# Performance work log

Measured on AMD Instinct MI355X. Metric: run time of the kernel, lower is better.

## Reference

```python
import jax, jax.numpy as jnp
import numpy as np

B, T, F = 128, 256, 6      # batch, input_seq_len, input feature dim
H, L = 512, 4              # hidden_size, hidden_layers
S, D = 32, 3               # output_seq_len, output_dim


def setup_inputs() -> dict:
    key = jax.random.key(0)
    ks = jax.random.split(key, 8)
    sc = 0.05
    x = jax.random.normal(ks[0], (B, T, F), dtype=jnp.float32)
    centre = jnp.zeros((F,), dtype=jnp.float32)          # uniform_centre
    bound = jnp.ones((F,), dtype=jnp.float32)            # uniform_bound
    W0 = jax.random.normal(ks[1], (F, 4 * H), dtype=jnp.float32) * sc   # layer0 kernel
    Wk = jax.random.normal(ks[2], (L - 1, H, 4 * H), dtype=jnp.float32) * sc  # layers 1..L-1 kernels
    U = jax.random.normal(ks[3], (L, H, 4 * H), dtype=jnp.float32) * sc # recurrent kernels
    b = jnp.zeros((L, 4 * H), dtype=jnp.float32)
    Wd = jax.random.normal(ks[4], (H, D), dtype=jnp.float32) * sc       # dense kernel
    bd = jnp.zeros((D,), dtype=jnp.float32)
    return {"x": x, "centre": centre, "bound": bound, "W0": W0,
            "Wk": Wk, "U": U, "b": b, "Wd": Wd, "bd": bd}


def _lstm_layer(x_tbf, W, U, b):
    """Keras LSTMCell over time-major input [T, B, Fin] -> [T, B, H]."""
    xW = jnp.einsum('tbf,fh->tbh', x_tbf, W)  # precompute input projections
    Bn = x_tbf.shape[1]
    Hn = U.shape[0]
    h0 = jnp.zeros((Bn, Hn), dtype=x_tbf.dtype)

    def step(carry, xw):
        h, c = carry
        z = xw + h @ U + b  # [B, 4H], keras gate order: i, f, g(c), o
        i, f, g, o = jnp.split(z, 4, axis=-1)
        i = jax.nn.sigmoid(i)
        f = jax.nn.sigmoid(f)
        g = jnp.tanh(g)
        o = jax.nn.sigmoid(o)
        c = f * c + i * g
        h = o * jnp.tanh(c)
        return (h, c), h

    _, hs = jax.lax.scan(step, (h0, h0), xW)
    return hs


def reference(x, centre, bound, W0, Wk, U, b, Wd, bd):
    # UniformDiff: uniform-scale then first difference along time (axis 1)
    u = (x - centre) / bound                 # [B, T, F]
    d = u[:, 1:, :] - u[:, :-1, :]           # [B, T-1, F]
    seq = jnp.transpose(d, (1, 0, 2))        # time-major [T-1, B, F]
    # stacked LSTM (generic RNN over StackedRNNCells)
    seq = _lstm_layer(seq, W0, U[0], b[0])
    for l in range(1, L):
        seq = _lstm_layer(seq, Wk[l - 1], U[l], b[l])
    h = jnp.transpose(seq, (1, 0, 2))        # [B, T-1, H]
    out = h[:, -S:, :] @ Wd + bd             # [B, S, D]
    # Restore: invert uniform scaling on the first D features
    pred = out * bound[:D] + centre[:D]
    return (out, pred)
```

## Files before the change

kernel.cpp:

```cpp
#include <hip/hip_runtime.h>
#include <cstdint>
#include <cstddef>


typedef __bf16 bf16x8  __attribute__((ext_vector_type(8)));
typedef float  f32x4   __attribute__((ext_vector_type(4)));
typedef float  f32x16  __attribute__((ext_vector_type(16)));
typedef unsigned int u32x4 __attribute__((ext_vector_type(4)));

#define STG_SLOT  262144ull
#define STG_L     65536ull
#define STG_MG    32768ull
#define STG_CG    1024ull

#define RING_SLOT 32768ull
#define RING_MG   (8ull*RING_SLOT)
#define RING_L    (2ull*RING_MG)
#define SZ_RING   (4ull*RING_L*2ull)

#define OFF_STG  0ull
#define SZ_STG   (256ull*STG_SLOT*2ull)
#define OFF_D    (OFF_STG + SZ_STG)
#define SZ_D     524288ull
#define OFF_BIAS (OFF_D + SZ_D)
#define SZ_BIAS  32768ull
#define OFF_FLAG (OFF_BIAS + SZ_BIAS)
#define SZ_FLAG  32768ull
#define OFF_FFLAG (OFF_FLAG + SZ_FLAG)
#define SZ_FFLAG 32768ull
#define OFF_RING (OFF_FFLAG + SZ_FFLAG)
#define OFF_BP   (OFF_RING + SZ_RING)
#define NK16_L0  33
#define BPE_L0   (64ull*NK16_L0*64ull*8ull)
#define BPE_STR  (64ull*64ull*64ull*8ull)

#define LDS_ZPAD   72
#define LDS_ZBYTES 18432
#define LDS_WBYTES 131072
#define LDS_TOTAL  (LDS_ZBYTES + LDS_WBYTES)

#define VMWAIT(N) do { asm volatile("s_waitcnt vmcnt(" #N ")" ::: "memory"); \
                       __builtin_amdgcn_sched_barrier(0); } while (0)

__device__ __forceinline__ void gld16(u32x4& d, const unsigned short* p) {
    asm volatile("global_load_dwordx4 %0, %1, off" : "=v"(d) : "v"(p));
}
__device__ __forceinline__ void gld16_sc0(u32x4& d, const unsigned short* p) {
    asm volatile("global_load_dwordx4 %0, %1, off sc0" : "=v"(d) : "v"(p));
}
__device__ __forceinline__ int ld_fast(const int* p) {
    int v;
    asm volatile("global_load_dword %0, %1, off sc0\n\t"
                 "s_waitcnt vmcnt(0)" : "=v"(v) : "v"(p) : "memory");
    return v;
}
__device__ __forceinline__ int ld_slow(const int* p) {
    return __hip_atomic_load(p, __ATOMIC_RELAXED, __HIP_MEMORY_SCOPE_AGENT);
}
__device__ __forceinline__ void ld_slow_async(int& v, const int* p) {
    asm volatile("global_load_dword %0, %1, off sc0 sc1" : "=v"(v) : "v"(p));
}

__device__ __forceinline__ unsigned short f2bf(float f) {
    unsigned int u = __builtin_bit_cast(unsigned int, f);
    unsigned int lsb = (u >> 16) & 1u;
    u += 0x7fffu + lsb;
    return (unsigned short)(u >> 16);
}
__device__ __forceinline__ float bf2f(unsigned short s) {
    unsigned int u = ((unsigned int)s) << 16;
    return __builtin_bit_cast(float, u);
}
__device__ __forceinline__ float fsig(float x)  { return 1.0f / (1.0f + __expf(-x)); }
__device__ __forceinline__ float ftanh(float x) { float e = __expf(2.0f * x); return 1.0f - 2.0f / (e + 1.0f); }

__global__ void prep_bias(const float* __restrict__ b, float* __restrict__ bias_ws) {
    int idx = blockIdx.x * 256 + threadIdx.x;
    if (idx >= 4 * 2048) return;
    int l = idx >> 11, c = idx & 2047;
    int j = ((c >> 6) << 4) + (c & 15);
    int gate = (c >> 4) & 3;
    bias_ws[idx] = b[l * 2048 + gate * 512 + j];
}

__global__ void prep_bp32(int layer, int NK16,
                          const float* __restrict__ W0, const float* __restrict__ Wk,
                          const float* __restrict__ U, unsigned short* __restrict__ bp) {
    int idx = blockIdx.x * 256 + threadIdx.x;
    int total = 64 * NK16 * 64;
    if (idx >= total) return;
    int lane = idx & 63;
    int rest = idx >> 6;
    int ks = rest % NK16;
    int ct = rest / NK16;
    int c = ct * 32 + (lane & 31);
    int j = ((c >> 6) << 4) + (c & 15);
    int gate = (c >> 4) & 3;
    int sc = gate * 512 + j;
    int kbase = ks * 16 + ((lane >> 5) << 3);
    unsigned short outv[8];
#pragma unroll
    for (int i = 0; i < 8; i++) {
        int k = kbase + i;
        float v = 0.0f;
        if (layer == 0) {
            if (k < 8) { if (k < 6) v = W0[(size_t)k * 2048 + sc]; }
            else if (k < 520) v = U[(size_t)(k - 8) * 2048 + sc];
        } else {
            if (k < 512) v = Wk[((size_t)(layer - 1) * 512 + k) * 2048 + sc];
            else         v = U[((size_t)layer * 512 + (k - 512)) * 2048 + sc];
        }
        outv[i] = f2bf(v);
    }
    *(uint4*)(bp + (size_t)idx * 8) = *(const uint4*)outv;
}

__global__ void diffk(const float* __restrict__ x, const float* __restrict__ bound,
                      unsigned short* __restrict__ dbuf) {
    int idx = blockIdx.x * 256 + threadIdx.x;
    if (idx >= 255 * 128) return;
    int item = idx & 127, t = idx >> 7;
    const float* xr = x + ((size_t)item * 256 + t) * 6;
    unsigned short row[8];
#pragma unroll
    for (int f = 0; f < 6; f++) row[f] = f2bf((xr[6 + f] - xr[f]) / bound[f]);
    row[6] = 0; row[7] = 0;
    *(uint4*)(dbuf + (size_t)idx * 8) = *(const uint4*)row;
}

__global__ __launch_bounds__(256, 1) void lstm_persist(
    const unsigned short* __restrict__ dbuf,
    unsigned short* __restrict__ stg,
    unsigned short* __restrict__ ring,
    const unsigned short* __restrict__ bp_all,
    const float* __restrict__ bias,
    int* __restrict__ slowf,
    int* __restrict__ fastf)
{
    extern __shared__ char smem[];
    float* zsm = (float*)smem;
    unsigned short* wsm = (unsigned short*)(smem + LDS_ZBYTES);

    (void)__hip_atomic_load(&slowf[0], __ATOMIC_ACQUIRE, __HIP_MEMORY_SCOPE_AGENT);

    const int blk   = blockIdx.x;
    const int stage = blk & 7;
    const int layer = stage >> 1;
    const int mg    = stage & 1;
    const int cg    = blk >> 3;
    const int tid   = threadIdx.x;
    const int w     = tid >> 6;
    const int lane  = tid & 63;
    const int NK16  = (layer == 0) ? NK16_L0 : 64;

    {
        const unsigned short* src = bp_all
            + (layer == 0 ? 0ull : (BPE_L0 + (size_t)(layer - 1) * BPE_STR))
            + (size_t)(cg * 2) * NK16 * 64 * 8;
        int nv = 2 * NK16 * 64;
        for (int e = tid; e < nv; e += 256)
            ((uint4*)wsm)[e] = ((const uint4*)src)[e];
    }
    __syncthreads();

    const int mt    = w >> 1;
    const int ntl   = w & 1;
    const int khalf = lane >> 5;
    const int arow  = mg * 64 + mt * 32 + (lane & 31);
    const int aloc  = arow & 63;
    const unsigned short* wbase = wsm + (size_t)ntl * NK16 * 512 + (size_t)lane * 8;
    const int citem = tid >> 2;
    const int jsub  = (tid & 3) << 2;
    const f32x4 bI = *(const f32x4*)(bias + layer * 2048 + cg * 64 + 0  + jsub);
    const f32x4 bF = *(const f32x4*)(bias + layer * 2048 + cg * 64 + 16 + jsub);
    const f32x4 bG = *(const f32x4*)(bias + layer * 2048 + cg * 64 + 32 + jsub);
    const f32x4 bO = *(const f32x4*)(bias + layer * 2048 + cg * 64 + 48 + jsub);

    const int own_base = stage * 32;
    const int lo_base  = (stage - 2) * 32;
    const int myfp     = (own_base + cg) * 32;
    const int pf       = lane & 31;
    const int ownfp    = (own_base + pf) * 32;
    const int lofp     = (lo_base + pf) * 32;

    unsigned short* ringW = ring + (size_t)layer * RING_L + (size_t)mg * RING_MG;
    const unsigned short* ringR = ringW;

    f32x4 creg = (f32x4){0.f, 0.f, 0.f, 0.f};

    int vlow = 0x7fffffff;
    if (layer > 0 && lane < 32) { ld_slow_async(vlow, &slowf[lofp]); }
    VMWAIT(0);

    for (int t = 0; t < 255; t++) {
        f32x16 c0 = {0.f,0.f,0.f,0.f,0.f,0.f,0.f,0.f,0.f,0.f,0.f,0.f,0.f,0.f,0.f,0.f};
        f32x16 c1 = c0, c2 = c0, c3 = c0;
        u32x4 A0[16], A1[16];

        auto consume = [&](u32x4 (&buf)[16], int wc0) {
#pragma unroll
            for (int j = 0; j < 16; j++) {
                int ch = wc0 + j;
                bf16x8 av = __builtin_bit_cast(bf16x8, buf[j]);
                bf16x8 bv = *(const bf16x8*)(wbase + (size_t)ch * 512);
                f32x16& cc = ((ch & 3) == 0) ? c0 : ((ch & 3) == 1) ? c1
                           : ((ch & 3) == 2) ? c2 : c3;
                cc = __builtin_amdgcn_mfma_f32_32x32x16_bf16(av, bv, cc, 0, 0, 0);
            }
        };

        auto own_poll = [&]() {
            for (;;) {
                int v = (lane < 32) ? ld_fast(&fastf[ownfp]) : 0x7fffffff;
                if (__all(v >= t)) break;
                if (lane < 32) { int v2 = ld_slow(&slowf[ownfp + 1]); v = v > v2 ? v : v2; }
                if (__all(v >= t)) break;
                __builtin_amdgcn_s_sleep(1);
            }
            __builtin_amdgcn_sched_barrier(0);
        };

        const unsigned short* rU = ringR + (size_t)(t & 7) * RING_SLOT
                                 + (size_t)aloc * 16 + (size_t)khalf * 8;

        if (layer == 0) {
            own_poll();
            const unsigned short* pD = dbuf + ((size_t)t * 128 + arow) * 8;
            auto issue0 = [&](u32x4 (&buf)[16], int kc0) {
#pragma unroll
                for (int j = 0; j < 16; j++) {
                    int kc = kc0 + j;
                    if (kc == 0 && khalf == 0) { gld16(buf[j], pD); }
                    else {
                        int hk = (kc * 16 + khalf * 8 - 8) & 511;
                        gld16_sc0(buf[j], ringR + (size_t)(t & 7) * RING_SLOT
                                  + (size_t)(hk >> 4) * STG_CG + (size_t)aloc * 16 + (hk & 15));
                    }
                }
            };
            issue0(A0, 0); issue0(A1, 16);
            VMWAIT(16); consume(A0, 0);
            {   int hk = (32 * 16 + khalf * 8 - 8) & 511;
                gld16_sc0(A0[0], ringR + (size_t)(t & 7) * RING_SLOT
                          + (size_t)(hk >> 4) * STG_CG + (size_t)aloc * 16 + (hk & 15)); }
            VMWAIT(1); consume(A1, 16);
            VMWAIT(0);
            {   bf16x8 av = __builtin_bit_cast(bf16x8, A0[0]);
                bf16x8 bv = *(const bf16x8*)(wbase + (size_t)32 * 512);
                c0 = __builtin_amdgcn_mfma_f32_32x32x16_bf16(av, bv, c0, 0, 0, 0); }
        } else {
            for (;;) {
                int v = (lane < 32) ? vlow : 0x7fffffff;
                if (__all(v >= t + 1)) break;
                __builtin_amdgcn_s_sleep(1);
                if (lane < 32) ld_slow_async(vlow, &slowf[lofp]);
                VMWAIT(0);
            }
            __builtin_amdgcn_sched_barrier(0);

            const unsigned short* aW = stg + (size_t)(t + 1) * STG_SLOT
                + (size_t)(layer - 1) * STG_L + (size_t)mg * STG_MG
                + (size_t)aloc * 16 + (size_t)khalf * 8;
#pragma unroll
            for (int j = 0; j < 16; j++) gld16(A0[j], aW + (size_t)j * STG_CG);
#pragma unroll
            for (int j = 0; j < 16; j++) gld16(A1[j], aW + (size_t)(16 + j) * STG_CG);
            VMWAIT(16); consume(A0, 0);
            VMWAIT(0);  consume(A1, 16);

            own_poll();

#pragma unroll
            for (int j = 0; j < 16; j++) gld16_sc0(A0[j], rU + (size_t)j * STG_CG);
#pragma unroll
            for (int j = 0; j < 16; j++) gld16_sc0(A1[j], rU + (size_t)(16 + j) * STG_CG);
            VMWAIT(16); consume(A0, 32);
            VMWAIT(0);  consume(A1, 48);
        }

        f32x16 acc = (c0 + c1) + (c2 + c3);

        {
            const int col   = ntl * 32 + (lane & 31);
            const int rbase = mt * 32 + 4 * khalf;
#pragma unroll
            for (int r = 0; r < 16; r++) {
                int row = rbase + (r & 3) + 8 * (r >> 2);
                zsm[row * LDS_ZPAD + col] = acc[r];
            }
        }
        __syncthreads();
        if (tid == 0 && t > 0)
            __hip_atomic_store(&slowf[myfp], t, __ATOMIC_RELAXED,
                               __HIP_MEMORY_SCOPE_AGENT);

        unsigned long long hpack;
        {
            const float* zr = zsm + citem * LDS_ZPAD + jsub;
            f32x4 zi = *(const f32x4*)(zr + 0);
            f32x4 zf = *(const f32x4*)(zr + 16);
            f32x4 zg = *(const f32x4*)(zr + 32);
            f32x4 zo = *(const f32x4*)(zr + 48);
            unsigned short hq[4];
#pragma unroll
            for (int q = 0; q < 4; q++) {
                float i_ = fsig(zi[q] + bI[q]);
                float f_ = fsig(zf[q] + bF[q]);
                float g_ = ftanh(zg[q] + bG[q]);
                float o_ = fsig(zo[q] + bO[q]);
                float cn = f_ * creg[q] + i_ * g_;
                creg[q] = cn;
                hq[q] = f2bf(o_ * ftanh(cn));
            }
            __builtin_memcpy(&hpack, hq, 8);
        }

        *(unsigned long long*)(ringW + (size_t)((t + 1) & 7) * RING_SLOT
            + (size_t)cg * STG_CG + (size_t)citem * 16 + jsub) = hpack;
        if (layer > 0 && lane < 32) ld_slow_async(vlow, &slowf[lofp]);
        __syncthreads();
        if (tid == 0) {
            int nv = t + 1;
            asm volatile("global_store_dword %0, %1, off sc0"
                         :: "v"(&fastf[myfp]), "v"(nv) : "memory");
            __hip_atomic_store(&slowf[myfp + 1], nv, __ATOMIC_RELAXED,
                               __HIP_MEMORY_SCOPE_AGENT);
        }

        {
            unsigned long long* hp = (unsigned long long*)(stg
                + (size_t)(t + 1) * STG_SLOT + (size_t)layer * STG_L
                + (size_t)mg * STG_MG + (size_t)cg * STG_CG
                + (size_t)citem * 16 + jsub);
            __hip_atomic_store(hp, hpack, __ATOMIC_RELAXED, __HIP_MEMORY_SCOPE_AGENT);
        }
    }

    asm volatile("s_waitcnt vmcnt(0)" ::: "memory");
    __syncthreads();
    if (tid == 0)
        __hip_atomic_store(&slowf[myfp], 255, __ATOMIC_RELAXED,
                           __HIP_MEMORY_SCOPE_AGENT);
}

__global__ void headk(const unsigned short* __restrict__ stg,
                      const float* __restrict__ Wd, const float* __restrict__ bd,
                      const float* __restrict__ bound, const float* __restrict__ centre,
                      float* __restrict__ out) {
    (void)__hip_atomic_load((const int*)stg, __ATOMIC_ACQUIRE, __HIP_MEMORY_SCOPE_AGENT);
    int idx = blockIdx.x * 256 + threadIdx.x;
    if (idx >= 12288) return;
    int dd = idx % 3;
    int rest = idx / 3;
    int sdx = rest & 31;
    int b = rest >> 5;
    size_t base = (size_t)(224 + sdx) * STG_SLOT + 3ull * STG_L
                + (size_t)(b >> 6) * STG_MG + (size_t)(b & 63) * 16;
    float acc = 0.0f;
    for (int jj = 0; jj < 512; jj++) {
        unsigned short hv = stg[base + (size_t)(jj >> 4) * STG_CG + (jj & 15)];
        acc += bf2f(hv) * Wd[jj * 3 + dd];
    }
    float o = acc + bd[dd];
    out[idx] = o;
    out[12288 + idx] = o * bound[dd] + centre[dd];
}

extern "C" void kernel_launch(void* const* d_in, const int* in_sizes, int n_in,
                              void* d_out, int out_size, void* d_ws, size_t ws_size,
                              hipStream_t stream) {
    const float* x      = (const float*)d_in[0];
    const float* centre = (const float*)d_in[1];
    const float* bound  = (const float*)d_in[2];
    const float* W0     = (const float*)d_in[3];
    const float* Wk     = (const float*)d_in[4];
    const float* U      = (const float*)d_in[5];
    const float* b      = (const float*)d_in[6];
    const float* Wd     = (const float*)d_in[7];
    const float* bd     = (const float*)d_in[8];

    char* ws = (char*)d_ws;
    unsigned short* stg     = (unsigned short*)(ws + OFF_STG);
    unsigned short* dbuf    = (unsigned short*)(ws + OFF_D);
    float*          bias_ws = (float*)(ws + OFF_BIAS);
    int*            slowf   = (int*)(ws + OFF_FLAG);
    int*            fastf   = (int*)(ws + OFF_FFLAG);
    unsigned short* ring    = (unsigned short*)(ws + OFF_RING);
    unsigned short* bp      = (unsigned short*)(ws + OFF_BP);

    (void)hipMemsetAsync(slowf, 0, SZ_FLAG + SZ_FFLAG + SZ_RING, stream);

    prep_bias<<<32, 256, 0, stream>>>(b, bias_ws);
    prep_bp32<<<528, 256, 0, stream>>>(0, NK16_L0, W0, Wk, U, bp);
    for (int l = 1; l < 4; l++)
        prep_bp32<<<1024, 256, 0, stream>>>(l, 64, W0, Wk, U,
                                            bp + BPE_L0 + (size_t)(l - 1) * BPE_STR);
    diffk<<<128, 256, 0, stream>>>(x, bound, dbuf);

    (void)hipFuncSetAttribute((const void*)lstm_persist,
                              hipFuncAttributeMaxDynamicSharedMemorySize, LDS_TOTAL);
    lstm_persist<<<256, 256, LDS_TOTAL, stream>>>(dbuf, stg, ring, bp, bias_ws,
                                                  slowf, fastf);

    headk<<<48, 256, 0, stream>>>(stg, Wd, bd, bound, centre, (float*)d_out);
}
```

Before: 1.444 ms.

## Prefetch next-step lower-layer input before the recurrent poll in layers above zero

For layers above zero, the wavefront now issues loads for the next timestep's input activations from the layer below at the end of the current step, when the lower layer's flag shows they are ready. It then waits on its own recurrent flag with those loads in flight. The A0/A1 register buffers are hoisted out of the loop so the prefetched data carries across iterations, and the staging area grows by one slot to cover the t+2 index. The __syncthreads calls for these layers become raw s_barrier with explicit waitcnts, so the prefetched loads need not drain at the first barrier. The cost is higher register pressure, and the first barrier now waits only on lgkmcnt, which is a subtle memory-ordering point.

```diff
diff --git a/kernel.cpp b/kernel.cpp
--- a/kernel.cpp
+++ b/kernel.cpp
@@ -19,7 +19,7 @@
 #define SZ_RING   (4ull*RING_L*2ull)
 
 #define OFF_STG  0ull
-#define SZ_STG   (256ull*STG_SLOT*2ull)
+#define SZ_STG   (257ull*STG_SLOT*2ull)
 #define OFF_D    (OFF_STG + SZ_STG)
 #define SZ_D     524288ull
 #define OFF_BIAS (OFF_D + SZ_D)
@@ -187,6 +187,8 @@
     const unsigned short* ringR = ringW;
 
     f32x4 creg = (f32x4){0.f, 0.f, 0.f, 0.f};
+    u32x4 A0[16], A1[16];
+    bool wpre = false;
 
     int vlow = 0x7fffffff;
     if (layer > 0 && lane < 32) { ld_slow_async(vlow, &slowf[lofp]); }
@@ -195,7 +197,6 @@
     for (int t = 0; t < 255; t++) {
         f32x16 c0 = {0.f,0.f,0.f,0.f,0.f,0.f,0.f,0.f,0.f,0.f,0.f,0.f,0.f,0.f,0.f,0.f};
         f32x16 c1 = c0, c2 = c0, c3 = c0;
-        u32x4 A0[16], A1[16];
 
         auto consume = [&](u32x4 (&buf)[16], int wc0) {
 #pragma unroll
@@ -249,27 +250,27 @@
                 bf16x8 bv = *(const bf16x8*)(wbase + (size_t)32 * 512);
                 c0 = __builtin_amdgcn_mfma_f32_32x32x16_bf16(av, bv, c0, 0, 0, 0); }
         } else {
-            for (;;) {
-                int v = (lane < 32) ? vlow : 0x7fffffff;
-                if (__all(v >= t + 1)) break;
-                __builtin_amdgcn_s_sleep(1);
-                if (lane < 32) ld_slow_async(vlow, &slowf[lofp]);
+            if (!wpre) {
                 VMWAIT(0);
-            }
-            __builtin_amdgcn_sched_barrier(0);
-
-            const unsigned short* aW = stg + (size_t)(t + 1) * STG_SLOT
-                + (size_t)(layer - 1) * STG_L + (size_t)mg * STG_MG
-                + (size_t)aloc * 16 + (size_t)khalf * 8;
-#pragma unroll
-            for (int j = 0; j < 16; j++) gld16(A0[j], aW + (size_t)j * STG_CG);
-#pragma unroll
-            for (int j = 0; j < 16; j++) gld16(A1[j], aW + (size_t)(16 + j) * STG_CG);
-            VMWAIT(16); consume(A0, 0);
-            VMWAIT(0);  consume(A1, 16);
-
+                for (;;) {
+                    int v = (lane < 32) ? vlow : 0x7fffffff;
+                    if (__all(v >= t + 1)) break;
+                    __builtin_amdgcn_s_sleep(1);
+                    if (lane < 32) ld_slow_async(vlow, &slowf[lofp]);
+                    VMWAIT(0);
+                }
+                __builtin_amdgcn_sched_barrier(0);
+                const unsigned short* aW = stg + (size_t)(t + 1) * STG_SLOT
+                    + (size_t)(layer - 1) * STG_L + (size_t)mg * STG_MG
+                    + (size_t)aloc * 16 + (size_t)khalf * 8;
+#pragma unroll
+                for (int j = 0; j < 16; j++) gld16(A0[j], aW + (size_t)j * STG_CG);
+#pragma unroll
+                for (int j = 0; j < 16; j++) gld16(A1[j], aW + (size_t)(16 + j) * STG_CG);
+            }
             own_poll();
-
+            consume(A0, 0);
+            consume(A1, 16);
 #pragma unroll
             for (int j = 0; j < 16; j++) gld16_sc0(A0[j], rU + (size_t)j * STG_CG);
 #pragma unroll
@@ -289,7 +290,14 @@
                 zsm[row * LDS_ZPAD + col] = acc[r];
             }
         }
-        __syncthreads();
+        if (layer == 0) {
+            __syncthreads();
+        } else {
+            asm volatile("s_waitcnt lgkmcnt(0)" ::: "memory");
+            __builtin_amdgcn_s_barrier();
+            asm volatile("" ::: "memory");
+            __builtin_amdgcn_sched_barrier(0);
+        }
         if (tid == 0 && t > 0)
             __hip_atomic_store(&slowf[myfp], t, __ATOMIC_RELAXED,
                                __HIP_MEMORY_SCOPE_AGENT);
@@ -317,8 +325,14 @@
 
         *(unsigned long long*)(ringW + (size_t)((t + 1) & 7) * RING_SLOT
             + (size_t)cg * STG_CG + (size_t)citem * 16 + jsub) = hpack;
-        if (layer > 0 && lane < 32) ld_slow_async(vlow, &slowf[lofp]);
-        __syncthreads();
+        if (layer == 0) {
+            __syncthreads();
+        } else {
+            asm volatile("s_waitcnt vmcnt(0)" ::: "memory");
+            __builtin_amdgcn_s_barrier();
+            asm volatile("" ::: "memory");
+            __builtin_amdgcn_sched_barrier(0);
+        }
         if (tid == 0) {
             int nv = t + 1;
             asm volatile("global_store_dword %0, %1, off sc0"
@@ -333,6 +347,24 @@
                 + (size_t)mg * STG_MG + (size_t)cg * STG_CG
                 + (size_t)citem * 16 + jsub);
             __hip_atomic_store(hp, hpack, __ATOMIC_RELAXED, __HIP_MEMORY_SCOPE_AGENT);
+        }
+
+        wpre = false;
+        if (layer > 0) {
+            if (t < 254) {
+                int v = (lane < 32) ? vlow : 0x7fffffff;
+                if (__all(v >= t + 2)) {
+                    const unsigned short* aW2 = stg + (size_t)(t + 2) * STG_SLOT
+                        + (size_t)(layer - 1) * STG_L + (size_t)mg * STG_MG
+                        + (size_t)aloc * 16 + (size_t)khalf * 8;
+#pragma unroll
+                    for (int j = 0; j < 16; j++) gld16(A0[j], aW2 + (size_t)j * STG_CG);
+#pragma unroll
+                    for (int j = 0; j < 16; j++) gld16(A1[j], aW2 + (size_t)(16 + j) * STG_CG);
+                    wpre = true;
+                }
+            }
+            if (lane < 32) ld_slow_async(vlow, &slowf[lofp]);
         }
     }
 
```

Measured after the change: 1.368 ms. 5.3% less time.
